# Performance work log

Measured on AMD Instinct MI355X. Metric: run time of the kernel, lower is better.

## Reference

```python
import jax, jax.numpy as jnp
import numpy as np

N_HEADS = 16

def setup_inputs() -> dict:
    key = jax.random.key(0)
    ks = jax.random.split(key, 6)
    B, S, D = 2, 2048, 1024
    return {
        "hidden_states": jax.random.normal(ks[0], (B, S, D), dtype=jnp.float32),
        "Wq": jax.random.normal(ks[1], (D, D), dtype=jnp.float32) * (1.0 / np.sqrt(D)),
        "Wk": jax.random.normal(ks[2], (D, D), dtype=jnp.float32) * (1.0 / np.sqrt(D)),
        "Wv": jax.random.normal(ks[3], (D, D), dtype=jnp.float32) * (1.0 / np.sqrt(D)),
        "Wo": jax.random.normal(ks[4], (D, D), dtype=jnp.float32) * (1.0 / np.sqrt(D)),
        "bo": jnp.zeros((D,), dtype=jnp.float32),
    }

def reference(hidden_states, Wq, Wk, Wv, Wo, bo):
    B, S, D = hidden_states.shape
    H = N_HEADS
    hd = D // H  # head_dim; d_kv == d_model per module's final view
    # nn.Linear(bias=False): x @ W.T, then the module's direct view to (B, H, S, hd)
    q = (hidden_states @ Wq.T).reshape(B, H, S, hd)
    k = (hidden_states @ Wk.T).reshape(B, H, S, hd)  # self-attention path (encoder_states=None)
    v = (hidden_states @ Wv.T).reshape(B, H, S, hd)
    # naive full score matrix [B, H, S, S]
    wei = jnp.einsum('bhqd,bhkd->bhqk', q, k)
    causal = jnp.tril(jnp.ones((S, S), dtype=bool))
    wei = jnp.where(causal, wei, -jnp.inf)
    # NOTE: module divides logits by head_dim (not sqrt) -- preserved faithfully
    attn = jax.nn.softmax(wei / hd, axis=-1)
    ctx = jnp.einsum('bhqk,bhkd->bhqd', attn, v)  # [B, H, S, hd]
    out = ctx.transpose(0, 2, 1, 3).reshape(B, S, D)
    return out @ Wo.T + bo
```

## Files before the change

kernel.cpp:

```cpp
#include <hip/hip_runtime.h>

#define S_LEN   2048
#define D_MODEL 1024
#define N_HEADS 16
#define HEAD_DIM 64

typedef unsigned short u16;
typedef float  floatx4 __attribute__((ext_vector_type(4)));
typedef short  bf16x8  __attribute__((ext_vector_type(8)));

__device__ __forceinline__ u16 f2bf(float f) {
    unsigned int u = __float_as_uint(f);
    u += 0x7FFF + ((u >> 16) & 1);
    return (u16)(u >> 16);
}
__device__ __forceinline__ unsigned pack2bf(float a, float b) {
    return (unsigned)f2bf(a) | ((unsigned)f2bf(b) << 16);
}

__device__ __forceinline__ void gload_lds16(const void* g, void* l) {
    __builtin_amdgcn_global_load_lds(
        reinterpret_cast<const __attribute__((address_space(1))) unsigned int*>(
            reinterpret_cast<uintptr_t>(g)),
        reinterpret_cast<__attribute__((address_space(3))) unsigned int*>(
            reinterpret_cast<uintptr_t>(l)),
        16, 0, 0);
}

__global__ __launch_bounds__(256) void cast_all(const float* __restrict__ hs,
                                                const float* __restrict__ w0,
                                                const float* __restrict__ w1,
                                                const float* __restrict__ w2,
                                                const float* __restrict__ w3,
                                                u16* __restrict__ dst) {
    const size_t NHS = (size_t)2 * S_LEN * D_MODEL;
    const size_t e0 = (size_t)blockIdx.x * 2048;
    const float* src;
    size_t base;
    if (e0 < NHS)                 { src = hs; base = 0; }
    else {
        const int wi = (int)((e0 - NHS) >> 20);
        src = wi == 0 ? w0 : wi == 1 ? w1 : wi == 2 ? w2 : w3;
        base = NHS + ((size_t)wi << 20);
    }
    const size_t i = e0 + (size_t)threadIdx.x * 8;
    const float4 a = *(const float4*)(src + (i - base));
    const float4 b = *(const float4*)(src + (i - base) + 4);
    uint4 o;
    o.x = pack2bf(a.x, a.y); o.y = pack2bf(a.z, a.w);
    o.z = pack2bf(b.x, b.y); o.w = pack2bf(b.z, b.w);
    *(uint4*)(dst + i) = o;
}

__global__ __launch_bounds__(256) void vtrans(const u16* __restrict__ Vf,
                                              u16* __restrict__ Vt) {
    __shared__ unsigned T[64 * 133];
    const int bh = blockIdx.y;
    const int sBase = blockIdx.x * 128;
    const u16* src = Vf + (size_t)bh * (S_LEN * HEAD_DIM) + (size_t)sBase * HEAD_DIM;
    u16* dst = Vt + (size_t)bh * (S_LEN * HEAD_DIM) + sBase;
    const int tid = threadIdx.x;

#pragma unroll
    for (int it = 0; it < 4; ++it) {
        const int idx = it * 256 + tid;
        const int row = idx >> 3, ch = idx & 7;
        const float4 v4 = *(const float4*)(src + row * 64 + ch * 8);
        const u16* vs = (const u16*)&v4;
#pragma unroll
        for (int j = 0; j < 8; ++j) T[(ch * 8 + j) * 133 + row] = vs[j];
    }
    __syncthreads();
#pragma unroll
    for (int it = 0; it < 4; ++it) {
        const int idx = it * 256 + tid;
        const int d = idx >> 4, sc = idx & 15;
        union { u16 u[8]; float4 f; } tmp;
#pragma unroll
        for (int j = 0; j < 8; ++j) tmp.u[j] = (u16)T[d * 133 + sc * 8 + j];
        *(float4*)(dst + (size_t)d * S_LEN + sc * 8) = tmp.f;
    }
}

__global__ __launch_bounds__(256) void gemm_qkv(const u16* __restrict__ A,
                                                const u16* __restrict__ Wq,
                                                const u16* __restrict__ Wk,
                                                const u16* __restrict__ Wv,
                                                u16* __restrict__ Qo,
                                                u16* __restrict__ Ko,
                                                u16* __restrict__ Vfo) {
    __shared__ u16 As[8 * 512];
    __shared__ u16 Ws[8 * 512];

    const int which = blockIdx.x >> 3;
    const int nBase = (blockIdx.x & 7) * 128;
    const int mBase = blockIdx.y * 128;
    const u16* W = which == 0 ? Wq : which == 1 ? Wk : Wv;

    const int tid = threadIdx.x, lane = tid & 63, wv = tid >> 6;
    const int l15 = lane & 15, quad = lane >> 4;
    const int wm = wv & 1, wn = wv >> 1;
    const int srow = lane >> 2;
    const int gch  = (lane & 3) ^ ((lane >> 3) & 3);
    const int swz  = (l15 >> 1) & 3;

    floatx4 acc[4][4];
#pragma unroll
    for (int i = 0; i < 4; ++i)
#pragma unroll
        for (int j = 0; j < 4; ++j) acc[i][j] = (floatx4)(0.0f);

    for (int k0 = 0; k0 < D_MODEL; k0 += 32) {
        __syncthreads();
#pragma unroll
        for (int t = 0; t < 2; ++t) {
            const int ci = wv * 2 + t;
            gload_lds16(A + (size_t)(mBase + ci * 16 + srow) * D_MODEL + k0 + gch * 8,
                        &As[ci * 512]);
            gload_lds16(W + (size_t)(nBase + ci * 16 + srow) * D_MODEL + k0 + gch * 8,
                        &Ws[ci * 512]);
        }
        __syncthreads();

        bf16x8 af[4], bfr[4];
#pragma unroll
        for (int mt = 0; mt < 4; ++mt)
            af[mt] = *(const bf16x8*)&As[(wm * 64 + mt * 16 + l15) * 32 + (quad ^ swz) * 8];
#pragma unroll
        for (int nt = 0; nt < 4; ++nt)
            bfr[nt] = *(const bf16x8*)&Ws[(wn * 64 + nt * 16 + l15) * 32 + (quad ^ swz) * 8];
#pragma unroll
        for (int mt = 0; mt < 4; ++mt)
#pragma unroll
            for (int nt = 0; nt < 4; ++nt)
                acc[mt][nt] = __builtin_amdgcn_mfma_f32_16x16x32_bf16(af[mt], bfr[nt], acc[mt][nt], 0, 0, 0);
    }

    u16* O = which == 0 ? Qo : (which == 1 ? Ko : Vfo);
    const float scale = which == 0 ? (1.44269504088896f / 64.0f) : 1.0f;
#pragma unroll
    for (int mt = 0; mt < 4; ++mt)
#pragma unroll
        for (int nt = 0; nt < 4; ++nt) {
            const int col = nBase + wn * 64 + nt * 16 + l15;
#pragma unroll
            for (int r = 0; r < 4; ++r) {
                const int row = mBase + wm * 64 + mt * 16 + quad * 4 + r;
                O[(size_t)row * D_MODEL + col] = f2bf(acc[mt][nt][r] * scale);
            }
        }
}

__global__ __launch_bounds__(256) void gemm_out(const u16* __restrict__ A,
                                                const u16* __restrict__ W,
                                                const float* __restrict__ bias,
                                                float* __restrict__ C) {
    __shared__ u16 As[4 * 512];
    __shared__ u16 Ws[8 * 512];

    const int nBase = blockIdx.x * 128;
    const int mBase = blockIdx.y * 64;
    const int tid = threadIdx.x, lane = tid & 63, wv = tid >> 6;
    const int l15 = lane & 15, quad = lane >> 4;
    const int wm = wv & 1, wn = wv >> 1;
    const int srow = lane >> 2;
    const int gch  = (lane & 3) ^ ((lane >> 3) & 3);
    const int swz  = (l15 >> 1) & 3;

    floatx4 acc[2][4];
#pragma unroll
    for (int i = 0; i < 2; ++i)
#pragma unroll
        for (int j = 0; j < 4; ++j) acc[i][j] = (floatx4)(0.0f);

    for (int k0 = 0; k0 < D_MODEL; k0 += 32) {
        __syncthreads();
        gload_lds16(A + (size_t)(mBase + wv * 16 + srow) * D_MODEL + k0 + gch * 8,
                    &As[wv * 512]);
#pragma unroll
        for (int t = 0; t < 2; ++t) {
            const int ci = wv * 2 + t;
            gload_lds16(W + (size_t)(nBase + ci * 16 + srow) * D_MODEL + k0 + gch * 8,
                        &Ws[ci * 512]);
        }
        __syncthreads();

        bf16x8 af[2], bfr[4];
#pragma unroll
        for (int mt = 0; mt < 2; ++mt)
            af[mt] = *(const bf16x8*)&As[(wm * 32 + mt * 16 + l15) * 32 + (quad ^ swz) * 8];
#pragma unroll
        for (int nt = 0; nt < 4; ++nt)
            bfr[nt] = *(const bf16x8*)&Ws[(wn * 64 + nt * 16 + l15) * 32 + (quad ^ swz) * 8];
#pragma unroll
        for (int mt = 0; mt < 2; ++mt)
#pragma unroll
            for (int nt = 0; nt < 4; ++nt)
                acc[mt][nt] = __builtin_amdgcn_mfma_f32_16x16x32_bf16(af[mt], bfr[nt], acc[mt][nt], 0, 0, 0);
    }

#pragma unroll
    for (int mt = 0; mt < 2; ++mt)
#pragma unroll
        for (int nt = 0; nt < 4; ++nt) {
            const int col = nBase + wn * 64 + nt * 16 + l15;
            const float bv = bias[col];
#pragma unroll
            for (int r = 0; r < 4; ++r) {
                const int row = mBase + wm * 32 + mt * 16 + quad * 4 + r;
                C[(size_t)row * D_MODEL + col] = acc[mt][nt][r] + bv;
            }
        }
}

__global__ __launch_bounds__(256) void attn3(const u16* __restrict__ Q,
                                             const u16* __restrict__ K,
                                             const u16* __restrict__ Vt,
                                             u16* __restrict__ Ctx) {
    __shared__ u16 Ks[2][8 * 512];
    __shared__ u16 Vs[2][8 * 512];
    __shared__ u16 Ps[4][16 * 72];

    const int flat = blockIdx.x;
    const int g    = (flat & 7) | ((flat >> 7) << 3);
    const int pair = (flat >> 3) & 15;
    const int h = g & 15, b = g >> 4;

    const int tid = threadIdx.x, lane = tid & 63, wv = tid >> 6;
    const int l15 = lane & 15, quad = lane >> 4;

    const size_t headOff = ((size_t)b * N_HEADS + h) * S_LEN * HEAD_DIM;
    const u16* Qh = Q + headOff;
    const u16* Kh = K + headOff;
    const u16* Vh = Vt + headOff;
    u16* Cb = Ctx + (size_t)b * S_LEN * D_MODEL + (size_t)h * HEAD_DIM;

    const int srow = lane >> 3;
    const int gch  = (lane & 7) ^ srow;
    const int swz  = l15 & 7;

    for (int half = 0; half < 2; ++half) {
        const int qt = half ? (31 - pair) : pair;
        const int qBase = qt * 64;

        bf16x8 qa[2];
#pragma unroll
        for (int ks = 0; ks < 2; ++ks)
            qa[ks] = *(const bf16x8*)(Qh + (size_t)(qBase + wv * 16 + l15) * 64 + ks * 32 + quad * 8);

        floatx4 o[4];
#pragma unroll
        for (int nt = 0; nt < 4; ++nt) o[nt] = (floatx4)(0.0f);
        float lp = 0.0f;

        __syncthreads();
#pragma unroll
        for (int t = 0; t < 2; ++t) {
            const int ci = wv * 2 + t;
            gload_lds16(Kh + (size_t)(ci * 8 + srow) * 64 + gch * 8, &Ks[0][ci * 512]);
            gload_lds16(Vh + (size_t)(ci * 8 + srow) * S_LEN + gch * 8, &Vs[0][ci * 512]);
        }

        int cur = 0;
        for (int kt = 0; kt <= qt; ++kt) {
            __syncthreads();
            if (kt < qt) {
                const int nb = (kt + 1) * 64;
#pragma unroll
                for (int t = 0; t < 2; ++t) {
                    const int ci = wv * 2 + t;
                    gload_lds16(Kh + (size_t)(nb + ci * 8 + srow) * 64 + gch * 8,
                                &Ks[cur ^ 1][ci * 512]);
                    gload_lds16(Vh + (size_t)(ci * 8 + srow) * S_LEN + nb + gch * 8,
                                &Vs[cur ^ 1][ci * 512]);
                }
            }

            floatx4 s[4];
#pragma unroll
            for (int mt = 0; mt < 4; ++mt) {
                s[mt] = (floatx4)(0.0f);
#pragma unroll
                for (int ks = 0; ks < 2; ++ks) {
                    const bf16x8 kb = *(const bf16x8*)&Ks[cur][(mt * 16 + l15) * 64 + ((ks * 4 + quad) ^ swz) * 8];
                    s[mt] = __builtin_amdgcn_mfma_f32_16x16x32_bf16(kb, qa[ks], s[mt], 0, 0, 0);
                }
            }

            const bool diag = (kt == qt);
#pragma unroll
            for (int mt = 0; mt < 4; ++mt) {
                float p[4];
#pragma unroll
                for (int r = 0; r < 4; ++r) {
                    float pv = exp2f(s[mt][r]);
                    if (diag && (mt * 16 + quad * 4 + r > wv * 16 + l15)) pv = 0.0f;
                    p[r] = pv;
                    lp += pv;
                }
                uint2 w;
                w.x = __builtin_amdgcn_perm(__float_as_uint(p[1]), __float_as_uint(p[0]), 0x07060302);
                w.y = __builtin_amdgcn_perm(__float_as_uint(p[3]), __float_as_uint(p[2]), 0x07060302);
                *(uint2*)&Ps[wv][l15 * 72 + mt * 16 + quad * 4] = w;
            }

            bf16x8 pa[2];
#pragma unroll
            for (int ks = 0; ks < 2; ++ks)
                pa[ks] = *(const bf16x8*)&Ps[wv][l15 * 72 + ks * 32 + quad * 8];
#pragma unroll
            for (int nt = 0; nt < 4; ++nt)
#pragma unroll
                for (int ks = 0; ks < 2; ++ks) {
                    const bf16x8 vb = *(const bf16x8*)&Vs[cur][(nt * 16 + l15) * 64 + ((ks * 4 + quad) ^ swz) * 8];
                    o[nt] = __builtin_amdgcn_mfma_f32_16x16x32_bf16(pa[ks], vb, o[nt], 0, 0, 0);
                }
            cur ^= 1;
        }

        lp += __shfl_xor(lp, 16);
        lp += __shfl_xor(lp, 32);

#pragma unroll
        for (int r = 0; r < 4; ++r) {
            const float inv = 1.0f / __shfl(lp, quad * 4 + r);
            const int row = qBase + wv * 16 + quad * 4 + r;
#pragma unroll
            for (int nt = 0; nt < 4; ++nt)
                Cb[(size_t)row * D_MODEL + nt * 16 + l15] = f2bf(o[nt][r] * inv);
        }
    }
}

extern "C" void kernel_launch(void* const* d_in, const int* in_sizes, int n_in,
                              void* d_out, int out_size, void* d_ws, size_t ws_size,
                              hipStream_t stream) {
    const float* hs = (const float*)d_in[0];
    const float* Wq = (const float*)d_in[1];
    const float* Wk = (const float*)d_in[2];
    const float* Wv = (const float*)d_in[3];
    const float* Wo = (const float*)d_in[4];
    const float* bo = (const float*)d_in[5];
    float* out = (float*)d_out;

    const size_t NHS = (size_t)2 * S_LEN * D_MODEL;
    const size_t NW  = (size_t)D_MODEL * D_MODEL;

    u16* hsb = (u16*)d_ws;
    u16* Wb  = hsb + NHS;
    u16* Qb  = Wb + 4 * NW;
    u16* Kb  = Qb + NHS;
    u16* Vfb = Kb + NHS;
    u16* Vtb = Vfb + NHS;
    u16* Cxb = Vtb + NHS;

    cast_all<<<4096, 256, 0, stream>>>(hs, Wq, Wk, Wv, Wo, hsb);

    gemm_qkv<<<dim3(24, 32), 256, 0, stream>>>(hsb, Wb, Wb + NW, Wb + 2 * NW,
                                               Qb, Kb, Vfb);

    vtrans<<<dim3(16, 32), 256, 0, stream>>>(Vfb, Vtb);

    attn3<<<512, 256, 0, stream>>>(Qb, Kb, Vtb, Cxb);

    gemm_out<<<dim3(8, 64), 256, 0, stream>>>(Cxb, Wb + 3 * NW, bo, out);
}
```

Measured before the change: 178.4 us.

## Split attention into one q-tile per block, drop K/V double buffering, remap QKV grid

The attention kernel now launches one block per (batch, head, q-tile), 1024 blocks in all, instead of pairing a short and a long q-tile in each of 512 blocks. Blocks are ordered longest-first so the causal work balances dynamically across CUs. The K/V LDS double buffer is replaced by a single buffer with load-then-sync, which halves LDS use and may raise occupancy but no longer overlaps loads with compute. The QKV GEMM grid is flattened and remapped so groups of consecutive blocks share weight tiles, improving L2 locality.

```diff
diff --git a/kernel.cpp b/kernel.cpp
--- a/kernel.cpp
+++ b/kernel.cpp
@@ -92,9 +92,12 @@
     __shared__ u16 As[8 * 512];
     __shared__ u16 Ws[8 * 512];
 
-    const int which = blockIdx.x >> 3;
-    const int nBase = (blockIdx.x & 7) * 128;
-    const int mBase = blockIdx.y * 128;
+    const int blk = blockIdx.x;
+    const int y   = (blk & 7) | (((blk >> 3) & 3) << 3);
+    const int x   = blk >> 5;
+    const int which = x >> 3;
+    const int nBase = (x & 7) * 128;
+    const int mBase = y * 128;
     const u16* W = which == 0 ? Wq : which == 1 ? Wk : Wv;
 
     const int tid = threadIdx.x, lane = tid & 63, wv = tid >> 6;
@@ -213,17 +216,17 @@
         }
 }
 
-__global__ __launch_bounds__(256) void attn3(const u16* __restrict__ Q,
+__global__ __launch_bounds__(256) void attn4(const u16* __restrict__ Q,
                                              const u16* __restrict__ K,
                                              const u16* __restrict__ Vt,
                                              u16* __restrict__ Ctx) {
-    __shared__ u16 Ks[2][8 * 512];
-    __shared__ u16 Vs[2][8 * 512];
+    __shared__ u16 Ks[8 * 512];
+    __shared__ u16 Vs[8 * 512];
     __shared__ u16 Ps[4][16 * 72];
 
     const int flat = blockIdx.x;
-    const int g    = (flat & 7) | ((flat >> 7) << 3);
-    const int pair = (flat >> 3) & 15;
+    const int g    = flat & 31;
+    const int qt   = 31 - (flat >> 5);
     const int h = g & 15, b = g >> 4;
 
     const int tid = threadIdx.x, lane = tid & 63, wv = tid >> 6;
@@ -239,96 +242,80 @@
     const int gch  = (lane & 7) ^ srow;
     const int swz  = l15 & 7;
 
-    for (int half = 0; half < 2; ++half) {
-        const int qt = half ? (31 - pair) : pair;
-        const int qBase = qt * 64;
-
-        bf16x8 qa[2];
-#pragma unroll
-        for (int ks = 0; ks < 2; ++ks)
-            qa[ks] = *(const bf16x8*)(Qh + (size_t)(qBase + wv * 16 + l15) * 64 + ks * 32 + quad * 8);
-
-        floatx4 o[4];
-#pragma unroll
-        for (int nt = 0; nt < 4; ++nt) o[nt] = (floatx4)(0.0f);
-        float lp = 0.0f;
-
+    const int qBase = qt * 64;
+
+    bf16x8 qa[2];
+#pragma unroll
+    for (int ks = 0; ks < 2; ++ks)
+        qa[ks] = *(const bf16x8*)(Qh + (size_t)(qBase + wv * 16 + l15) * 64 + ks * 32 + quad * 8);
+
+    floatx4 o[4];
+#pragma unroll
+    for (int nt = 0; nt < 4; ++nt) o[nt] = (floatx4)(0.0f);
+    float lp = 0.0f;
+
+    for (int kt = 0; kt <= qt; ++kt) {
+        const int kBase = kt * 64;
         __syncthreads();
 #pragma unroll
         for (int t = 0; t < 2; ++t) {
             const int ci = wv * 2 + t;
-            gload_lds16(Kh + (size_t)(ci * 8 + srow) * 64 + gch * 8, &Ks[0][ci * 512]);
-            gload_lds16(Vh + (size_t)(ci * 8 + srow) * S_LEN + gch * 8, &Vs[0][ci * 512]);
-        }
-
-        int cur = 0;
-        for (int kt = 0; kt <= qt; ++kt) {
-            __syncthreads();
-            if (kt < qt) {
-                const int nb = (kt + 1) * 64;
-#pragma unroll
-                for (int t = 0; t < 2; ++t) {
-                    const int ci = wv * 2 + t;
-                    gload_lds16(Kh + (size_t)(nb + ci * 8 + srow) * 64 + gch * 8,
-                                &Ks[cur ^ 1][ci * 512]);
-                    gload_lds16(Vh + (size_t)(ci * 8 + srow) * S_LEN + nb + gch * 8,
-                                &Vs[cur ^ 1][ci * 512]);
-                }
-            }
-
-            floatx4 s[4];
-#pragma unroll
-            for (int mt = 0; mt < 4; ++mt) {
-                s[mt] = (floatx4)(0.0f);
-#pragma unroll
-                for (int ks = 0; ks < 2; ++ks) {
-                    const bf16x8 kb = *(const bf16x8*)&Ks[cur][(mt * 16 + l15) * 64 + ((ks * 4 + quad) ^ swz) * 8];
-                    s[mt] = __builtin_amdgcn_mfma_f32_16x16x32_bf16(kb, qa[ks], s[mt], 0, 0, 0);
-                }
-            }
-
-            const bool diag = (kt == qt);
-#pragma unroll
-            for (int mt = 0; mt < 4; ++mt) {
-                float p[4];
-#pragma unroll
-                for (int r = 0; r < 4; ++r) {
-                    float pv = exp2f(s[mt][r]);
-                    if (diag && (mt * 16 + quad * 4 + r > wv * 16 + l15)) pv = 0.0f;
-                    p[r] = pv;
-                    lp += pv;
-                }
-                uint2 w;
-                w.x = __builtin_amdgcn_perm(__float_as_uint(p[1]), __float_as_uint(p[0]), 0x07060302);
-                w.y = __builtin_amdgcn_perm(__float_as_uint(p[3]), __float_as_uint(p[2]), 0x07060302);
-                *(uint2*)&Ps[wv][l15 * 72 + mt * 16 + quad * 4] = w;
-            }
-
-            bf16x8 pa[2];
-#pragma unroll
-            for (int ks = 0; ks < 2; ++ks)
-                pa[ks] = *(const bf16x8*)&Ps[wv][l15 * 72 + ks * 32 + quad * 8];
-#pragma unroll
-            for (int nt = 0; nt < 4; ++nt)
-#pragma unroll
-                for (int ks = 0; ks < 2; ++ks) {
-                    const bf16x8 vb = *(const bf16x8*)&Vs[cur][(nt * 16 + l15) * 64 + ((ks * 4 + quad) ^ swz) * 8];
-                    o[nt] = __builtin_amdgcn_mfma_f32_16x16x32_bf16(pa[ks], vb, o[nt], 0, 0, 0);
-                }
-            cur ^= 1;
-        }
-
-        lp += __shfl_xor(lp, 16);
-        lp += __shfl_xor(lp, 32);
-
-#pragma unroll
-        for (int r = 0; r < 4; ++r) {
-            const float inv = 1.0f / __shfl(lp, quad * 4 + r);
-            const int row = qBase + wv * 16 + quad * 4 + r;
-#pragma unroll
-            for (int nt = 0; nt < 4; ++nt)
-                Cb[(size_t)row * D_MODEL + nt * 16 + l15] = f2bf(o[nt][r] * inv);
-        }
+            gload_lds16(Kh + (size_t)(kBase + ci * 8 + srow) * 64 + gch * 8, &Ks[ci * 512]);
+            gload_lds16(Vh + (size_t)(ci * 8 + srow) * S_LEN + kBase + gch * 8, &Vs[ci * 512]);
+        }
+        __syncthreads();
+
+        floatx4 s[4];
+#pragma unroll
+        for (int mt = 0; mt < 4; ++mt) {
+            s[mt] = (floatx4)(0.0f);
+#pragma unroll
+            for (int ks = 0; ks < 2; ++ks) {
+                const bf16x8 kb = *(const bf16x8*)&Ks[(mt * 16 + l15) * 64 + ((ks * 4 + quad) ^ swz) * 8];
+                s[mt] = __builtin_amdgcn_mfma_f32_16x16x32_bf16(kb, qa[ks], s[mt], 0, 0, 0);
+            }
+        }
+
+        const bool diag = (kt == qt);
+#pragma unroll
+        for (int mt = 0; mt < 4; ++mt) {
+            float p[4];
+#pragma unroll
+            for (int r = 0; r < 4; ++r) {
+                float pv = exp2f(s[mt][r]);
+                if (diag && (mt * 16 + quad * 4 + r > wv * 16 + l15)) pv = 0.0f;
+                p[r] = pv;
+                lp += pv;
+            }
+            uint2 w;
+            w.x = __builtin_amdgcn_perm(__float_as_uint(p[1]), __float_as_uint(p[0]), 0x07060302);
+            w.y = __builtin_amdgcn_perm(__float_as_uint(p[3]), __float_as_uint(p[2]), 0x07060302);
+            *(uint2*)&Ps[wv][l15 * 72 + mt * 16 + quad * 4] = w;
+        }
+
+        bf16x8 pa[2];
+#pragma unroll
+        for (int ks = 0; ks < 2; ++ks)
+            pa[ks] = *(const bf16x8*)&Ps[wv][l15 * 72 + ks * 32 + quad * 8];
+#pragma unroll
+        for (int nt = 0; nt < 4; ++nt)
+#pragma unroll
+            for (int ks = 0; ks < 2; ++ks) {
+                const bf16x8 vb = *(const bf16x8*)&Vs[(nt * 16 + l15) * 64 + ((ks * 4 + quad) ^ swz) * 8];
+                o[nt] = __builtin_amdgcn_mfma_f32_16x16x32_bf16(pa[ks], vb, o[nt], 0, 0, 0);
+            }
+    }
+
+    lp += __shfl_xor(lp, 16);
+    lp += __shfl_xor(lp, 32);
+
+#pragma unroll
+    for (int r = 0; r < 4; ++r) {
+        const float inv = 1.0f / __shfl(lp, quad * 4 + r);
+        const int row = qBase + wv * 16 + quad * 4 + r;
+#pragma unroll
+        for (int nt = 0; nt < 4; ++nt)
+            Cb[(size_t)row * D_MODEL + nt * 16 + l15] = f2bf(o[nt][r] * inv);
     }
 }
 
@@ -356,12 +343,12 @@
 
     cast_all<<<4096, 256, 0, stream>>>(hs, Wq, Wk, Wv, Wo, hsb);
 
-    gemm_qkv<<<dim3(24, 32), 256, 0, stream>>>(hsb, Wb, Wb + NW, Wb + 2 * NW,
-                                               Qb, Kb, Vfb);
+    gemm_qkv<<<768, 256, 0, stream>>>(hsb, Wb, Wb + NW, Wb + 2 * NW,
+                                      Qb, Kb, Vfb);
 
     vtrans<<<dim3(16, 32), 256, 0, stream>>>(Vfb, Vtb);
 
-    attn3<<<512, 256, 0, stream>>>(Qb, Kb, Vtb, Cxb);
+    attn4<<<1024, 256, 0, stream>>>(Qb, Kb, Vtb, Cxb);
 
     gemm_out<<<dim3(8, 64), 256, 0, stream>>>(Cxb, Wb + 3 * NW, bo, out);
 }
```

After: 181.4 us. No clear change (+1.6%).
